# Performance work log

Measured on AMD Instinct MI355X. Metric: run time of the kernel, lower is better.

Reference implementation:

```python
import jax, jax.numpy as jnp
import numpy as np

V, E, H, N, B, T_CAP = 10000, 2048, 512, 98, 32, 61


def setup_inputs() -> dict:
    key = jax.random.key(0)
    ks = jax.random.split(key, 24)
    p = lambda k, shape: jax.random.normal(k, shape, dtype=jnp.float32) * 0.02
    inp = {
        "img_features": jax.random.normal(ks[0], (B, N, E), dtype=jnp.float32),
        "captions": jax.random.randint(ks[1], (B, T_CAP), 0, V),
        "emb": p(ks[2], (V, H)),
        "W_init_h": p(ks[3], (H, E)), "b_init_h": jnp.zeros((H,), jnp.float32),
        "W_init_c": p(ks[4], (H, E)), "b_init_c": jnp.zeros((H,), jnp.float32),
        "W_U": p(ks[5], (H, H)), "b_U": jnp.zeros((H,), jnp.float32),
        "W_att": p(ks[6], (H, E)), "b_att": jnp.zeros((H,), jnp.float32),
        "W_v": p(ks[7], (1, H)), "b_v": jnp.zeros((1,), jnp.float32),
        "W_fb": p(ks[8], (E, H)), "b_fb": jnp.zeros((E,), jnp.float32),
        "W_ih": p(ks[9], (4 * H, H + E)), "b_ih": jnp.zeros((4 * H,), jnp.float32),
        "W_hh": p(ks[10], (4 * H, H)), "b_hh": jnp.zeros((4 * H,), jnp.float32),
        "W_out": p(ks[11], (V, H)), "b_out": jnp.zeros((V,), jnp.float32),
    }
    return inp


def reference(img_features, captions, emb, W_init_h, b_init_h, W_init_c, b_init_c,
              W_U, b_U, W_att, b_att, W_v, b_v, W_fb, b_fb,
              W_ih, b_ih, W_hh, b_hh, W_out, b_out):
    # training-mode forward: max_timespan = caption_len - 1; dropout as identity (eval-style determinism)
    T = captions.shape[1] - 1
    avg = img_features.mean(axis=1)  # [B, E]
    h = jnp.tanh(avg @ W_init_h.T + b_init_h)  # [B, H]
    c = jnp.tanh(avg @ W_init_c.T + b_init_c)
    # Embeddings with sqrt(d_model) scaling
    emb_seq = emb[captions] * jnp.sqrt(jnp.float32(emb.shape[1]))  # [B, T_cap, H]
    # W_s is timestep-invariant: hoist out of loop (same math)
    Ws = jnp.einsum('bne,he->bnh', img_features, W_att) + b_att  # [B, N, H]

    def step(carry, emb_t):
        h, c = carry
        att = jnp.tanh(Ws + (h @ W_U.T + b_U)[:, None, :])       # [B, N, H]
        e = jnp.einsum('bnh,h->bn', att, W_v[0]) + b_v[0]        # [B, N]
        alpha = jax.nn.softmax(e, axis=1)
        context = jnp.einsum('bne,bn->be', img_features, alpha)  # [B, E]
        gate = jax.nn.sigmoid(h @ W_fb.T + b_fb)                 # [B, E]
        x = jnp.concatenate([emb_t, gate * context], axis=1)     # [B, H+E]
        gates = x @ W_ih.T + b_ih + h @ W_hh.T + b_hh            # [B, 4H]
        i_, f_, g_, o_ = jnp.split(gates, 4, axis=1)             # torch LSTMCell gate order
        c2 = jax.nn.sigmoid(f_) * c + jax.nn.sigmoid(i_) * jnp.tanh(g_)
        h2 = jax.nn.sigmoid(o_) * jnp.tanh(c2)
        pred = h2 @ W_out.T + b_out                              # [B, V]
        return (h2, c2), pred

    emb_steps = jnp.swapaxes(emb_seq[:, :T], 0, 1)  # [T, B, H]
    (_, _), preds = jax.lax.scan(step, (h, c), emb_steps)
    return jnp.swapaxes(preds, 0, 1)  # [B, T, V]
```

## Files before the change

### kernel.cpp

```cpp
#include <hip/hip_runtime.h>
#include <hip/hip_bf16.h>

#define BB   32
#define NN   98
#define EE   2048
#define HH   512
#define VV   10000
#define TT   60
#define TCAP 61

typedef unsigned short u16;
typedef __attribute__((ext_vector_type(8))) short bh8;
typedef __attribute__((ext_vector_type(4))) float f32x4;

__device__ __forceinline__ float bsf(unsigned s) {
    union { unsigned u; float f; } w; w.u = s << 16; return w.f;
}
__device__ __forceinline__ u16 f2bu(float f) {
    union { float f; unsigned u; } v; v.f = f;
    unsigned u = v.u;
    u = u + 0x7fffu + ((u >> 16) & 1u);
    return (u16)(u >> 16);
}
__device__ __forceinline__ bh8 ld8(const u16* p) {
    return *reinterpret_cast<const bh8*>(p);
}
__device__ __forceinline__ float sigm(float x) {
    return __builtin_amdgcn_rcpf(1.0f + exp2f(-1.4426950408889634f * x));
}
__device__ __forceinline__ float tanh_(float x) {
    return 1.0f - 2.0f * __builtin_amdgcn_rcpf(1.0f + exp2f(2.885390081777927f * x));
}

__global__ __launch_bounds__(256) void k_conv(
    const float* __restrict__ src, u16* __restrict__ dst)
{
    int i = blockIdx.x * 256 + threadIdx.x;
    float4 v = reinterpret_cast<const float4*>(src)[i];
    ushort4 o;
    o.x = f2bu(v.x); o.y = f2bu(v.y); o.z = f2bu(v.z); o.w = f2bu(v.w);
    reinterpret_cast<ushort4*>(dst)[i] = o;
}

__global__ __launch_bounds__(256) void k_init1(
    const float* __restrict__ img, const int* __restrict__ caps,
    const float* __restrict__ emb, u16* __restrict__ avg_bf, u16* __restrict__ emb_all)
{
    int bid = blockIdx.x, tid = threadIdx.x;
    if (bid < 256) {
        int b = bid >> 3, et = bid & 7;
        int ec = et * 256 + tid;
        const float* p = img + (size_t)(b * NN) * EE + ec;
        float s = 0.f;
        for (int n = 0; n < NN; ++n) s += p[(size_t)n * EE];
        avg_bf[b * EE + ec] = f2bu(s * (1.0f / 98.0f));
    } else {
        int eb = bid - 256;
        for (int r8 = 0; r8 < 8; ++r8) {
            int row = eb * 8 + r8;
            int t = row >> 5, b = row & 31;
            int cap = caps[b * TCAP + t];
            const float* src = emb + (size_t)cap * HH;
            u16* dst = emb_all + (size_t)row * HH;
            for (int c = tid; c < HH; c += 256)
                dst[c] = f2bu(src[c] * 22.627416997969522f);
        }
    }
}

__global__ __launch_bounds__(256) void k_init2(
    const u16* __restrict__ avg_bf,
    const u16* __restrict__ Wh_bf, const float* __restrict__ b_h,
    const u16* __restrict__ Wc_bf, const float* __restrict__ b_c,
    u16* __restrict__ h_all, float* __restrict__ c_ws)
{
    __shared__ float red[4][2][64][4];
    int ot = blockIdx.x, tid = threadIdx.x;
    int w = tid >> 6, lane = tid & 63, quad = lane >> 4, l16 = lane & 15;
    int o = ot * 16 + l16;
    const u16* wrow = (o < HH) ? (Wh_bf + (size_t)o * EE) : (Wc_bf + (size_t)(o - HH) * EE);
    f32x4 acc[2]; acc[0] = {0,0,0,0}; acc[1] = {0,0,0,0};
    for (int c = w * 16; c < w * 16 + 16; ++c) {
        int k = c * 32 + quad * 8;
        bh8 b8 = ld8(wrow + k);
        for (int mt = 0; mt < 2; ++mt) {
            bh8 a8 = ld8(avg_bf + (size_t)(mt * 16 + l16) * EE + k);
            acc[mt] = __builtin_amdgcn_mfma_f32_16x16x32_bf16(a8, b8, acc[mt], 0, 0, 0);
        }
    }
    for (int mt = 0; mt < 2; ++mt)
        for (int r = 0; r < 4; ++r) red[w][mt][lane][r] = acc[mt][r];
    __syncthreads();
    for (int idx = tid; idx < 512; idx += 256) {
        int mg = idx >> 4, nn2 = idx & 15;
        int mt = mg >> 4, m = mg & 15;
        int sl = nn2 + 16 * (m >> 2), rg = m & 3;
        float v = red[0][mt][sl][rg] + red[1][mt][sl][rg] + red[2][mt][sl][rg] + red[3][mt][sl][rg];
        int oo = ot * 16 + nn2, b = mg;
        if (oo < HH)
            h_all[(size_t)b * HH + oo] = f2bu(tanh_(v + b_h[oo]));
        else
            c_ws[b * HH + (oo - HH)] = tanh_(v + b_c[oo - HH]);
    }
}

__global__ __launch_bounds__(256) void k_ws(
    const u16* __restrict__ img_bf, const u16* __restrict__ Watt_bf,
    const float* __restrict__ b_att, u16* __restrict__ Ws_bf)
{
    int bid = blockIdx.x, tid = threadIdx.x;
    int mt = bid >> 4, nt = bid & 15;
    int w = tid >> 6, lane = tid & 63, quad = lane >> 4, l16 = lane & 15;
    int rowA = mt * 64 + w * 16 + l16;
    f32x4 acc[2]; acc[0] = {0,0,0,0}; acc[1] = {0,0,0,0};
    const u16* arow = img_bf + (size_t)rowA * EE;
    for (int c = 0; c < 64; ++c) {
        int k = c * 32 + quad * 8;
        bh8 a8 = ld8(arow + k);
        for (int s = 0; s < 2; ++s) {
            bh8 b8 = ld8(Watt_bf + (size_t)(nt * 32 + s * 16 + l16) * EE + k);
            acc[s] = __builtin_amdgcn_mfma_f32_16x16x32_bf16(a8, b8, acc[s], 0, 0, 0);
        }
    }
    for (int s = 0; s < 2; ++s)
        for (int r = 0; r < 4; ++r) {
            int m = quad * 4 + r;
            int row = mt * 64 + w * 16 + m;
            int col = nt * 32 + s * 16 + l16;
            Ws_bf[(size_t)row * HH + col] = f2bu(acc[s][r] + b_att[col]);
        }
}

__global__ __launch_bounds__(256) void k_c(
    const u16* __restrict__ h_all, int tIn,
    const u16* __restrict__ WU_bf, const float* __restrict__ b_U,
    const u16* __restrict__ Wfb_bf, const float* __restrict__ b_fb,
    float* __restrict__ Wu_ws, float* __restrict__ gate_ws)
{
    __shared__ float red[4][2][64][4];
    int ot = blockIdx.x, tid = threadIdx.x;
    int w = tid >> 6, lane = tid & 63, quad = lane >> 4, l16 = lane & 15;
    int o = ot * 16 + l16;
    const u16* wrow = (o < HH) ? (WU_bf + (size_t)o * HH) : (Wfb_bf + (size_t)(o - HH) * HH);
    const u16* hbase = h_all + (size_t)tIn * BB * HH;
    f32x4 acc[2]; acc[0] = {0,0,0,0}; acc[1] = {0,0,0,0};
    for (int c = w * 4; c < w * 4 + 4; ++c) {
        int k = c * 32 + quad * 8;
        bh8 b8 = ld8(wrow + k);
        for (int mt = 0; mt < 2; ++mt) {
            bh8 a8 = ld8(hbase + (size_t)(mt * 16 + l16) * HH + k);
            acc[mt] = __builtin_amdgcn_mfma_f32_16x16x32_bf16(a8, b8, acc[mt], 0, 0, 0);
        }
    }
    for (int mt = 0; mt < 2; ++mt)
        for (int r = 0; r < 4; ++r) red[w][mt][lane][r] = acc[mt][r];
    __syncthreads();
    for (int idx = tid; idx < 512; idx += 256) {
        int mg = idx >> 4, nn2 = idx & 15;
        int mt = mg >> 4, m = mg & 15;
        int sl = nn2 + 16 * (m >> 2), rg = m & 3;
        float v = red[0][mt][sl][rg] + red[1][mt][sl][rg] + red[2][mt][sl][rg] + red[3][mt][sl][rg];
        int oo = ot * 16 + nn2, b = mg;
        if (oo < HH)
            Wu_ws[b * HH + oo] = v + b_U[oo];
        else
            gate_ws[b * EE + (oo - HH)] = sigm(v + b_fb[oo - HH]);
    }
}

__global__ __launch_bounds__(256) void k_a(
    const float* __restrict__ img, const u16* __restrict__ Ws_bf,
    const float* __restrict__ Wu_ws, const float* __restrict__ gate_ws,
    const float* __restrict__ W_v, const float* __restrict__ b_v,
    u16* __restrict__ xctx)
{
    __shared__ float e_sh[NN];
    __shared__ float a_sh[NN];
    int bid = blockIdx.x, tid = threadIdx.x;
    int b = bid >> 2, et = bid & 3;
    int w = tid >> 6, lane = tid & 63;
    float wu[8], wv[8];
    {
        const float* wup = Wu_ws + b * HH + lane * 8;
        const float* wvp = W_v + lane * 8;
        #pragma unroll
        for (int j = 0; j < 8; ++j) { wu[j] = wup[j]; wv[j] = wvp[j]; }
    }
    for (int n = w; n < NN; n += 4) {
        bh8 ws8 = ld8(Ws_bf + (size_t)(b * NN + n) * HH + lane * 8);
        float acc = 0.f;
        #pragma unroll
        for (int j = 0; j < 8; ++j) acc += wv[j] * tanh_(bsf((u16)ws8[j]) + wu[j]);
        #pragma unroll
        for (int off = 32; off > 0; off >>= 1) acc += __shfl_down(acc, off, 64);
        if (lane == 0) e_sh[n] = acc + b_v[0];
    }
    __syncthreads();
    if (tid < 64) {
        float e0 = e_sh[tid];
        float e1 = (tid + 64 < NN) ? e_sh[tid + 64] : -1e30f;
        float m = fmaxf(e0, e1);
        #pragma unroll
        for (int off = 32; off > 0; off >>= 1) m = fmaxf(m, __shfl_xor(m, off, 64));
        const float L2E = 1.4426950408889634f;
        float x0 = exp2f((e0 - m) * L2E);
        float x1 = (tid + 64 < NN) ? exp2f((e1 - m) * L2E) : 0.f;
        float s = x0 + x1;
        #pragma unroll
        for (int off = 32; off > 0; off >>= 1) s += __shfl_xor(s, off, 64);
        float inv = __builtin_amdgcn_rcpf(s);
        a_sh[tid] = x0 * inv;
        if (tid + 64 < NN) a_sh[tid + 64] = x1 * inv;
    }
    __syncthreads();
    int ec = et * 512 + tid * 2;
    const float* ip = img + (size_t)b * NN * EE + ec;
    float c0 = 0.f, c1 = 0.f;
    for (int n = 0; n < NN; ++n) {
        float2 u = *reinterpret_cast<const float2*>(ip + (size_t)n * EE);
        float a = a_sh[n];
        c0 = fmaf(a, u.x, c0); c1 = fmaf(a, u.y, c1);
    }
    float g0 = gate_ws[b * EE + ec], g1 = gate_ws[b * EE + ec + 1];
    unsigned outw = ((unsigned)f2bu(g1 * c1) << 16) | (unsigned)f2bu(g0 * c0);
    *reinterpret_cast<unsigned*>(xctx + (size_t)b * EE + ec) = outw;
}

__global__ __launch_bounds__(256) void k_b(
    int t,
    const u16* __restrict__ emb_all, const u16* __restrict__ xctx,
    u16* h_all,
    const u16* __restrict__ Wih_bf, const float* __restrict__ b_ih,
    const u16* __restrict__ Whh_bf, const float* __restrict__ b_hh,
    float* __restrict__ c_ws)
{
    __shared__ float red[4][64][4];
    __shared__ float gsh[16][16];
    int bid = blockIdx.x, tid = threadIdx.x;
    int kt = bid & 127, mt = bid >> 7;
    int w = tid >> 6, lane = tid & 63, quad = lane >> 4, l16 = lane & 15;
    int brow = mt * 16 + l16;
    int j = kt * 4 + (l16 & 3) + HH * (l16 >> 2);
    const u16* embrow = emb_all + (size_t)(t * BB + brow) * HH;
    const u16* xrow   = xctx + (size_t)brow * EE;
    const u16* hrow   = h_all + (size_t)(t * BB + brow) * HH;
    const u16* wih    = Wih_bf + (size_t)j * (HH + EE);
    const u16* whh    = Whh_bf + (size_t)j * HH;
    f32x4 acc = {0,0,0,0};
    for (int c = w * 24; c < w * 24 + 24; ++c) {
        int k = c * 32 + quad * 8;
        bh8 a8, b8;
        if (c < 16)      a8 = ld8(embrow + k);
        else if (c < 80) a8 = ld8(xrow + (k - HH));
        else             a8 = ld8(hrow + (k - HH - EE));
        if (c < 80)      b8 = ld8(wih + k);
        else             b8 = ld8(whh + (k - HH - EE));
        acc = __builtin_amdgcn_mfma_f32_16x16x32_bf16(a8, b8, acc, 0, 0, 0);
    }
    for (int r = 0; r < 4; ++r) red[w][lane][r] = acc[r];
    __syncthreads();
    {
        int m = tid >> 4, nn2 = tid & 15;
        int sl = nn2 + 16 * (m >> 2), rg = m & 3;
        int jj = kt * 4 + (nn2 & 3) + HH * (nn2 >> 2);
        float v = red[0][sl][rg] + red[1][sl][rg] + red[2][sl][rg] + red[3][sl][rg]
                + b_ih[jj] + b_hh[jj];
        gsh[m][nn2] = v;
    }
    __syncthreads();
    if (tid < 64) {
        int m = tid >> 2, i = tid & 3;
        int b = mt * 16 + m, k = kt * 4 + i;
        float gi = gsh[m][i], gf = gsh[m][i + 4], gg = gsh[m][i + 8], go = gsh[m][i + 12];
        float cold = c_ws[b * HH + k];
        float c2 = sigm(gf) * cold + sigm(gi) * tanh_(gg);
        float h2 = sigm(go) * tanh_(c2);
        c_ws[b * HH + k] = c2;
        h_all[(size_t)((t + 1) * BB + b) * HH + k] = f2bu(h2);
    }
}

__global__ __launch_bounds__(256) void k_pred(
    const u16* __restrict__ h_all, const u16* __restrict__ Wout_bf,
    const float* __restrict__ b_out, float* __restrict__ out)
{
    int bid = blockIdx.x, tid = threadIdx.x;
    int mt = bid / 79, vt = bid % 79;
    int w = tid >> 6, lane = tid & 63, quad = lane >> 4, l16 = lane & 15;
    f32x4 acc[8][2];
    for (int mi = 0; mi < 8; ++mi) for (int s = 0; s < 2; ++s) acc[mi][s] = {0,0,0,0};
    int nact[2]; int vbase[2];
    for (int s = 0; s < 2; ++s) {
        int ntg = vt * 8 + 2 * w + s;
        nact[s] = (ntg < 625);
        vbase[s] = ntg * 16;
    }
    for (int c = 0; c < 16; ++c) {
        int k = c * 32 + quad * 8;
        bh8 b8[2];
        for (int s = 0; s < 2; ++s) if (nact[s])
            b8[s] = ld8(Wout_bf + (size_t)(vbase[s] + l16) * HH + k);
        for (int mi = 0; mi < 8; ++mi) {
            int row = 32 + mt * 128 + mi * 16 + l16;
            bh8 a8 = ld8(h_all + (size_t)row * HH + k);
            for (int s = 0; s < 2; ++s) if (nact[s])
                acc[mi][s] = __builtin_amdgcn_mfma_f32_16x16x32_bf16(a8, b8[s], acc[mi][s], 0, 0, 0);
        }
    }
    for (int s = 0; s < 2; ++s) if (nact[s]) {
        int v = vbase[s] + l16;
        float bo = b_out[v];
        for (int mi = 0; mi < 8; ++mi)
            for (int r = 0; r < 4; ++r) {
                int row = 32 + mt * 128 + mi * 16 + quad * 4 + r;
                int tt = (row >> 5) - 1, b = row & 31;
                out[(size_t)(b * TT + tt) * VV + v] = acc[mi][s][r] + bo;
            }
    }
}

extern "C" void kernel_launch(void* const* d_in, const int* in_sizes, int n_in,
                              void* d_out, int out_size, void* d_ws, size_t ws_size,
                              hipStream_t stream)
{
    const float* img      = (const float*)d_in[0];
    const int*   caps     = (const int*)d_in[1];
    const float* emb      = (const float*)d_in[2];
    const float* W_init_h = (const float*)d_in[3];
    const float* b_init_h = (const float*)d_in[4];
    const float* W_init_c = (const float*)d_in[5];
    const float* b_init_c = (const float*)d_in[6];
    const float* W_U      = (const float*)d_in[7];
    const float* b_U      = (const float*)d_in[8];
    const float* W_att    = (const float*)d_in[9];
    const float* b_att    = (const float*)d_in[10];
    const float* W_v      = (const float*)d_in[11];
    const float* b_v      = (const float*)d_in[12];
    const float* W_fb     = (const float*)d_in[13];
    const float* b_fb     = (const float*)d_in[14];
    const float* W_ih     = (const float*)d_in[15];
    const float* b_ih     = (const float*)d_in[16];
    const float* W_hh     = (const float*)d_in[17];
    const float* b_hh     = (const float*)d_in[18];
    const float* W_out    = (const float*)d_in[19];
    const float* b_out    = (const float*)d_in[20];
    float* out = (float*)d_out;

    char* ws = (char*)d_ws;
    u16*   img_bf  = (u16*)(ws);
    u16*   Watt_bf = (u16*)(ws + 12845056);
    u16*   Winh_bf = (u16*)(ws + 14942208);
    u16*   Winc_bf = (u16*)(ws + 17039360);
    u16*   WU_bf   = (u16*)(ws + 19136512);
    u16*   Wfb_bf  = (u16*)(ws + 19660800);
    u16*   Wih_bf  = (u16*)(ws + 21757952);
    u16*   Whh_bf  = (u16*)(ws + 32243712);
    u16*   Wout_bf = (u16*)(ws + 34340864);
    u16*   Ws_bf   = (u16*)(ws + 44580864);
    u16*   emb_all = (u16*)(ws + 47792128);
    u16*   h_all   = (u16*)(ws + 49758208);
    u16*   xctx    = (u16*)(ws + 51757056);
    u16*   avg_bf  = (u16*)(ws + 51888128);
    float* c_ws    = (float*)(ws + 52019200);
    float* Wu_ws   = (float*)(ws + 52084736);
    float* gate_ws = (float*)(ws + 52150272);

    k_conv<<<6272, 256, 0, stream>>>(img,      img_bf);
    k_conv<<<1024, 256, 0, stream>>>(W_att,    Watt_bf);
    k_conv<<<1024, 256, 0, stream>>>(W_init_h, Winh_bf);
    k_conv<<<1024, 256, 0, stream>>>(W_init_c, Winc_bf);
    k_conv<<< 256, 256, 0, stream>>>(W_U,      WU_bf);
    k_conv<<<1024, 256, 0, stream>>>(W_fb,     Wfb_bf);
    k_conv<<<5120, 256, 0, stream>>>(W_ih,     Wih_bf);
    k_conv<<<1024, 256, 0, stream>>>(W_hh,     Whh_bf);
    k_conv<<<5000, 256, 0, stream>>>(W_out,    Wout_bf);

    k_init1<<<496, 256, 0, stream>>>(img, caps, emb, avg_bf, emb_all);
    k_init2<<<64, 256, 0, stream>>>(avg_bf, Winh_bf, b_init_h, Winc_bf, b_init_c, h_all, c_ws);
    k_ws<<<784, 256, 0, stream>>>(img_bf, Watt_bf, b_att, Ws_bf);
    k_c<<<160, 256, 0, stream>>>(h_all, 0, WU_bf, b_U, Wfb_bf, b_fb, Wu_ws, gate_ws);
    for (int t = 0; t < TT; ++t) {
        k_a<<<128, 256, 0, stream>>>(img, Ws_bf, Wu_ws, gate_ws, W_v, b_v, xctx);
        k_b<<<256, 256, 0, stream>>>(t, emb_all, xctx, h_all, Wih_bf, b_ih, Whh_bf, b_hh, c_ws);
        if (t < TT - 1)
            k_c<<<160, 256, 0, stream>>>(h_all, t + 1, WU_bf, b_U, Wfb_bf, b_fb, Wu_ws, gate_ws);
    }
    k_pred<<<1185, 256, 0, stream>>>(h_all, Wout_bf, b_out, out);
}
```

Before: 2.669 ms.

## Fuse recurrent timestep kernels into one persistent kernel with grid barriers

Replaces the 179 per-timestep launches of k_a, k_b and k_c with a single persistent kernel of 256 blocks. The phases are separated by a software grid barrier built on an atomic counter and spin-waiting. The aim is to remove per-launch overhead and the gaps between launches on the sequential recurrence. In exchange it relies on all 256 blocks being co-resident, which needs 256 blocks on the GPU, and on correct memory fences; any block that is not resident would deadlock.

```diff
diff --git a/kernel.cpp b/kernel.cpp
--- a/kernel.cpp
+++ b/kernel.cpp
@@ -8,6 +8,7 @@
 #define VV   10000
 #define TT   60
 #define TCAP 61
+#define NBLK 256
 
 typedef unsigned short u16;
 typedef __attribute__((ext_vector_type(8))) short bh8;
@@ -131,152 +132,186 @@
         }
 }
 
-__global__ __launch_bounds__(256) void k_c(
-    const u16* __restrict__ h_all, int tIn,
+__global__ void k_zero(unsigned* cnt) { if (threadIdx.x == 0) *cnt = 0u; }
+
+__device__ __forceinline__ void gsync(unsigned* cnt, unsigned target) {
+    __syncthreads();
+    if (threadIdx.x == 0) {
+        __threadfence();
+        __hip_atomic_fetch_add(cnt, 1u, __ATOMIC_RELAXED, __HIP_MEMORY_SCOPE_AGENT);
+        unsigned v;
+        do {
+            __builtin_amdgcn_s_sleep(1);
+            v = __hip_atomic_load(cnt, __ATOMIC_RELAXED, __HIP_MEMORY_SCOPE_AGENT);
+        } while (v < target);
+        __threadfence();
+    }
+    __syncthreads();
+}
+
+__global__ __launch_bounds__(256, 2) void k_loop(
+    const float* __restrict__ img,
+    const u16* __restrict__ Ws_bf,
+    float* __restrict__ Wu_ws, float* __restrict__ gate_ws,
+    const float* __restrict__ W_v, const float* __restrict__ b_v,
+    u16* __restrict__ xctx,
+    const u16* __restrict__ emb_all,
+    u16* __restrict__ h_all,
+    const u16* __restrict__ Wih_bf, const float* __restrict__ b_ih,
+    const u16* __restrict__ Whh_bf, const float* __restrict__ b_hh,
+    float* __restrict__ c_ws,
     const u16* __restrict__ WU_bf, const float* __restrict__ b_U,
     const u16* __restrict__ Wfb_bf, const float* __restrict__ b_fb,
-    float* __restrict__ Wu_ws, float* __restrict__ gate_ws)
-{
-    __shared__ float red[4][2][64][4];
-    int ot = blockIdx.x, tid = threadIdx.x;
-    int w = tid >> 6, lane = tid & 63, quad = lane >> 4, l16 = lane & 15;
-    int o = ot * 16 + l16;
-    const u16* wrow = (o < HH) ? (WU_bf + (size_t)o * HH) : (Wfb_bf + (size_t)(o - HH) * HH);
-    const u16* hbase = h_all + (size_t)tIn * BB * HH;
-    f32x4 acc[2]; acc[0] = {0,0,0,0}; acc[1] = {0,0,0,0};
-    for (int c = w * 4; c < w * 4 + 4; ++c) {
-        int k = c * 32 + quad * 8;
-        bh8 b8 = ld8(wrow + k);
-        for (int mt = 0; mt < 2; ++mt) {
-            bh8 a8 = ld8(hbase + (size_t)(mt * 16 + l16) * HH + k);
-            acc[mt] = __builtin_amdgcn_mfma_f32_16x16x32_bf16(a8, b8, acc[mt], 0, 0, 0);
-        }
-    }
-    for (int mt = 0; mt < 2; ++mt)
-        for (int r = 0; r < 4; ++r) red[w][mt][lane][r] = acc[mt][r];
-    __syncthreads();
-    for (int idx = tid; idx < 512; idx += 256) {
-        int mg = idx >> 4, nn2 = idx & 15;
-        int mt = mg >> 4, m = mg & 15;
-        int sl = nn2 + 16 * (m >> 2), rg = m & 3;
-        float v = red[0][mt][sl][rg] + red[1][mt][sl][rg] + red[2][mt][sl][rg] + red[3][mt][sl][rg];
-        int oo = ot * 16 + nn2, b = mg;
-        if (oo < HH)
-            Wu_ws[b * HH + oo] = v + b_U[oo];
-        else
-            gate_ws[b * EE + (oo - HH)] = sigm(v + b_fb[oo - HH]);
-    }
-}
-
-__global__ __launch_bounds__(256) void k_a(
-    const float* __restrict__ img, const u16* __restrict__ Ws_bf,
-    const float* __restrict__ Wu_ws, const float* __restrict__ gate_ws,
-    const float* __restrict__ W_v, const float* __restrict__ b_v,
-    u16* __restrict__ xctx)
-{
+    unsigned* cnt)
+{
+    __shared__ float redC[4][2][64][4];
+    __shared__ float redB[4][64][4];
+    __shared__ float gsh[16][16];
     __shared__ float e_sh[NN];
     __shared__ float a_sh[NN];
-    int bid = blockIdx.x, tid = threadIdx.x;
-    int b = bid >> 2, et = bid & 3;
-    int w = tid >> 6, lane = tid & 63;
-    float wu[8], wv[8];
-    {
-        const float* wup = Wu_ws + b * HH + lane * 8;
-        const float* wvp = W_v + lane * 8;
-        #pragma unroll
-        for (int j = 0; j < 8; ++j) { wu[j] = wup[j]; wv[j] = wvp[j]; }
-    }
-    for (int n = w; n < NN; n += 4) {
-        bh8 ws8 = ld8(Ws_bf + (size_t)(b * NN + n) * HH + lane * 8);
-        float acc = 0.f;
-        #pragma unroll
-        for (int j = 0; j < 8; ++j) acc += wv[j] * tanh_(bsf((u16)ws8[j]) + wu[j]);
-        #pragma unroll
-        for (int off = 32; off > 0; off >>= 1) acc += __shfl_down(acc, off, 64);
-        if (lane == 0) e_sh[n] = acc + b_v[0];
-    }
-    __syncthreads();
-    if (tid < 64) {
-        float e0 = e_sh[tid];
-        float e1 = (tid + 64 < NN) ? e_sh[tid + 64] : -1e30f;
-        float m = fmaxf(e0, e1);
-        #pragma unroll
-        for (int off = 32; off > 0; off >>= 1) m = fmaxf(m, __shfl_xor(m, off, 64));
-        const float L2E = 1.4426950408889634f;
-        float x0 = exp2f((e0 - m) * L2E);
-        float x1 = (tid + 64 < NN) ? exp2f((e1 - m) * L2E) : 0.f;
-        float s = x0 + x1;
-        #pragma unroll
-        for (int off = 32; off > 0; off >>= 1) s += __shfl_xor(s, off, 64);
-        float inv = __builtin_amdgcn_rcpf(s);
-        a_sh[tid] = x0 * inv;
-        if (tid + 64 < NN) a_sh[tid + 64] = x1 * inv;
-    }
-    __syncthreads();
-    int ec = et * 512 + tid * 2;
-    const float* ip = img + (size_t)b * NN * EE + ec;
-    float c0 = 0.f, c1 = 0.f;
-    for (int n = 0; n < NN; ++n) {
-        float2 u = *reinterpret_cast<const float2*>(ip + (size_t)n * EE);
-        float a = a_sh[n];
-        c0 = fmaf(a, u.x, c0); c1 = fmaf(a, u.y, c1);
-    }
-    float g0 = gate_ws[b * EE + ec], g1 = gate_ws[b * EE + ec + 1];
-    unsigned outw = ((unsigned)f2bu(g1 * c1) << 16) | (unsigned)f2bu(g0 * c0);
-    *reinterpret_cast<unsigned*>(xctx + (size_t)b * EE + ec) = outw;
-}
-
-__global__ __launch_bounds__(256) void k_b(
-    int t,
-    const u16* __restrict__ emb_all, const u16* __restrict__ xctx,
-    u16* h_all,
-    const u16* __restrict__ Wih_bf, const float* __restrict__ b_ih,
-    const u16* __restrict__ Whh_bf, const float* __restrict__ b_hh,
-    float* __restrict__ c_ws)
-{
-    __shared__ float red[4][64][4];
-    __shared__ float gsh[16][16];
-    int bid = blockIdx.x, tid = threadIdx.x;
-    int kt = bid & 127, mt = bid >> 7;
-    int w = tid >> 6, lane = tid & 63, quad = lane >> 4, l16 = lane & 15;
-    int brow = mt * 16 + l16;
-    int j = kt * 4 + (l16 & 3) + HH * (l16 >> 2);
-    const u16* embrow = emb_all + (size_t)(t * BB + brow) * HH;
-    const u16* xrow   = xctx + (size_t)brow * EE;
-    const u16* hrow   = h_all + (size_t)(t * BB + brow) * HH;
-    const u16* wih    = Wih_bf + (size_t)j * (HH + EE);
-    const u16* whh    = Whh_bf + (size_t)j * HH;
-    f32x4 acc = {0,0,0,0};
-    for (int c = w * 24; c < w * 24 + 24; ++c) {
-        int k = c * 32 + quad * 8;
-        bh8 a8, b8;
-        if (c < 16)      a8 = ld8(embrow + k);
-        else if (c < 80) a8 = ld8(xrow + (k - HH));
-        else             a8 = ld8(hrow + (k - HH - EE));
-        if (c < 80)      b8 = ld8(wih + k);
-        else             b8 = ld8(whh + (k - HH - EE));
-        acc = __builtin_amdgcn_mfma_f32_16x16x32_bf16(a8, b8, acc, 0, 0, 0);
-    }
-    for (int r = 0; r < 4; ++r) red[w][lane][r] = acc[r];
-    __syncthreads();
-    {
-        int m = tid >> 4, nn2 = tid & 15;
-        int sl = nn2 + 16 * (m >> 2), rg = m & 3;
-        int jj = kt * 4 + (nn2 & 3) + HH * (nn2 >> 2);
-        float v = red[0][sl][rg] + red[1][sl][rg] + red[2][sl][rg] + red[3][sl][rg]
-                + b_ih[jj] + b_hh[jj];
-        gsh[m][nn2] = v;
-    }
-    __syncthreads();
-    if (tid < 64) {
-        int m = tid >> 2, i = tid & 3;
-        int b = mt * 16 + m, k = kt * 4 + i;
-        float gi = gsh[m][i], gf = gsh[m][i + 4], gg = gsh[m][i + 8], go = gsh[m][i + 12];
-        float cold = c_ws[b * HH + k];
-        float c2 = sigm(gf) * cold + sigm(gi) * tanh_(gg);
-        float h2 = sigm(go) * tanh_(c2);
-        c_ws[b * HH + k] = c2;
-        h_all[(size_t)((t + 1) * BB + b) * HH + k] = f2bu(h2);
+
+    const int bid = blockIdx.x, tid = threadIdx.x;
+    const int w = tid >> 6, lane = tid & 63, quad = lane >> 4, l16 = lane & 15;
+    unsigned snc = 0;
+
+    auto phaseC = [&](int tIn) {
+        if (bid < 160) {
+            int ot = bid;
+            int o = ot * 16 + l16;
+            const u16* wrow = (o < HH) ? (WU_bf + (size_t)o * HH) : (Wfb_bf + (size_t)(o - HH) * HH);
+            const u16* hbase = h_all + (size_t)tIn * BB * HH;
+            f32x4 acc[2]; acc[0] = {0,0,0,0}; acc[1] = {0,0,0,0};
+            for (int c = w * 4; c < w * 4 + 4; ++c) {
+                int k = c * 32 + quad * 8;
+                bh8 b8 = ld8(wrow + k);
+                for (int mt = 0; mt < 2; ++mt) {
+                    bh8 a8 = ld8(hbase + (size_t)(mt * 16 + l16) * HH + k);
+                    acc[mt] = __builtin_amdgcn_mfma_f32_16x16x32_bf16(a8, b8, acc[mt], 0, 0, 0);
+                }
+            }
+            for (int mt = 0; mt < 2; ++mt)
+                for (int r = 0; r < 4; ++r) redC[w][mt][lane][r] = acc[mt][r];
+            __syncthreads();
+            for (int idx = tid; idx < 512; idx += 256) {
+                int mg = idx >> 4, nn2 = idx & 15;
+                int mt = mg >> 4, m = mg & 15;
+                int sl = nn2 + 16 * (m >> 2), rg = m & 3;
+                float v = redC[0][mt][sl][rg] + redC[1][mt][sl][rg]
+                        + redC[2][mt][sl][rg] + redC[3][mt][sl][rg];
+                int oo = ot * 16 + nn2, b = mg;
+                if (oo < HH)
+                    Wu_ws[b * HH + oo] = v + b_U[oo];
+                else
+                    gate_ws[b * EE + (oo - HH)] = sigm(v + b_fb[oo - HH]);
+            }
+        }
+    };
+
+    auto phaseA = [&]() {
+        if (bid < 128) {
+            int b = bid >> 2, et = bid & 3;
+            float wu[8], wv[8];
+            {
+                const float* wup = Wu_ws + b * HH + lane * 8;
+                const float* wvp = W_v + lane * 8;
+                #pragma unroll
+                for (int j = 0; j < 8; ++j) { wu[j] = wup[j]; wv[j] = wvp[j]; }
+            }
+            for (int n = w; n < NN; n += 4) {
+                bh8 ws8 = ld8(Ws_bf + (size_t)(b * NN + n) * HH + lane * 8);
+                float acc = 0.f;
+                #pragma unroll
+                for (int j = 0; j < 8; ++j) acc += wv[j] * tanh_(bsf((u16)ws8[j]) + wu[j]);
+                #pragma unroll
+                for (int off = 32; off > 0; off >>= 1) acc += __shfl_down(acc, off, 64);
+                if (lane == 0) e_sh[n] = acc + b_v[0];
+            }
+            __syncthreads();
+            if (tid < 64) {
+                float e0 = e_sh[tid];
+                float e1 = (tid + 64 < NN) ? e_sh[tid + 64] : -1e30f;
+                float m = fmaxf(e0, e1);
+                #pragma unroll
+                for (int off = 32; off > 0; off >>= 1) m = fmaxf(m, __shfl_xor(m, off, 64));
+                const float L2E = 1.4426950408889634f;
+                float x0 = exp2f((e0 - m) * L2E);
+                float x1 = (tid + 64 < NN) ? exp2f((e1 - m) * L2E) : 0.f;
+                float s = x0 + x1;
+                #pragma unroll
+                for (int off = 32; off > 0; off >>= 1) s += __shfl_xor(s, off, 64);
+                float inv = __builtin_amdgcn_rcpf(s);
+                a_sh[tid] = x0 * inv;
+                if (tid + 64 < NN) a_sh[tid + 64] = x1 * inv;
+            }
+            __syncthreads();
+            int ec = et * 512 + tid * 2;
+            const float* ip = img + (size_t)b * NN * EE + ec;
+            float c0 = 0.f, c1 = 0.f;
+            for (int n = 0; n < NN; ++n) {
+                float2 u = *reinterpret_cast<const float2*>(ip + (size_t)n * EE);
+                float a = a_sh[n];
+                c0 = fmaf(a, u.x, c0); c1 = fmaf(a, u.y, c1);
+            }
+            float g0 = gate_ws[b * EE + ec], g1 = gate_ws[b * EE + ec + 1];
+            unsigned outw = ((unsigned)f2bu(g1 * c1) << 16) | (unsigned)f2bu(g0 * c0);
+            *reinterpret_cast<unsigned*>(xctx + (size_t)b * EE + ec) = outw;
+        }
+    };
+
+    auto phaseB = [&](int t) {
+        int kt = bid & 127, mt = bid >> 7;
+        int brow = mt * 16 + l16;
+        int j = kt * 4 + (l16 & 3) + HH * (l16 >> 2);
+        const u16* embrow = emb_all + (size_t)(t * BB + brow) * HH;
+        const u16* xrow   = xctx + (size_t)brow * EE;
+        const u16* hrow   = h_all + (size_t)(t * BB + brow) * HH;
+        const u16* wih    = Wih_bf + (size_t)j * (HH + EE);
+        const u16* whh    = Whh_bf + (size_t)j * HH;
+        f32x4 acc = {0,0,0,0};
+        for (int c = w * 24; c < w * 24 + 24; ++c) {
+            int k = c * 32 + quad * 8;
+            bh8 a8, b8;
+            if (c < 16)      a8 = ld8(embrow + k);
+            else if (c < 80) a8 = ld8(xrow + (k - HH));
+            else             a8 = ld8(hrow + (k - HH - EE));
+            if (c < 80)      b8 = ld8(wih + k);
+            else             b8 = ld8(whh + (k - HH - EE));
+            acc = __builtin_amdgcn_mfma_f32_16x16x32_bf16(a8, b8, acc, 0, 0, 0);
+        }
+        for (int r = 0; r < 4; ++r) redB[w][lane][r] = acc[r];
+        __syncthreads();
+        {
+            int m = tid >> 4, nn2 = tid & 15;
+            int sl = nn2 + 16 * (m >> 2), rg = m & 3;
+            int jj = kt * 4 + (nn2 & 3) + HH * (nn2 >> 2);
+            float v = redB[0][sl][rg] + redB[1][sl][rg] + redB[2][sl][rg] + redB[3][sl][rg]
+                    + b_ih[jj] + b_hh[jj];
+            gsh[m][nn2] = v;
+        }
+        __syncthreads();
+        if (tid < 64) {
+            int m = tid >> 2, i = tid & 3;
+            int b = mt * 16 + m, k = kt * 4 + i;
+            float gi = gsh[m][i], gf = gsh[m][i + 4], gg = gsh[m][i + 8], go = gsh[m][i + 12];
+            float cold = c_ws[b * HH + k];
+            float c2 = sigm(gf) * cold + sigm(gi) * tanh_(gg);
+            float h2 = sigm(go) * tanh_(c2);
+            c_ws[b * HH + k] = c2;
+            h_all[(size_t)((t + 1) * BB + b) * HH + k] = f2bu(h2);
+        }
+    };
+
+    phaseC(0);
+    gsync(cnt, ++snc * NBLK);
+    for (int t = 0; t < TT; ++t) {
+        phaseA();
+        gsync(cnt, ++snc * NBLK);
+        phaseB(t);
+        gsync(cnt, ++snc * NBLK);
+        if (t < TT - 1) {
+            phaseC(t + 1);
+            gsync(cnt, ++snc * NBLK);
+        }
     }
 }
 
@@ -364,6 +399,7 @@
     float* c_ws    = (float*)(ws + 52019200);
     float* Wu_ws   = (float*)(ws + 52084736);
     float* gate_ws = (float*)(ws + 52150272);
+    unsigned* sync_cnt = (unsigned*)(ws + 52412416);
 
     k_conv<<<6272, 256, 0, stream>>>(img,      img_bf);
     k_conv<<<1024, 256, 0, stream>>>(W_att,    Watt_bf);
@@ -378,12 +414,11 @@
     k_init1<<<496, 256, 0, stream>>>(img, caps, emb, avg_bf, emb_all);
     k_init2<<<64, 256, 0, stream>>>(avg_bf, Winh_bf, b_init_h, Winc_bf, b_init_c, h_all, c_ws);
     k_ws<<<784, 256, 0, stream>>>(img_bf, Watt_bf, b_att, Ws_bf);
-    k_c<<<160, 256, 0, stream>>>(h_all, 0, WU_bf, b_U, Wfb_bf, b_fb, Wu_ws, gate_ws);
-    for (int t = 0; t < TT; ++t) {
-        k_a<<<128, 256, 0, stream>>>(img, Ws_bf, Wu_ws, gate_ws, W_v, b_v, xctx);
-        k_b<<<256, 256, 0, stream>>>(t, emb_all, xctx, h_all, Wih_bf, b_ih, Whh_bf, b_hh, c_ws);
-        if (t < TT - 1)
-            k_c<<<160, 256, 0, stream>>>(h_all, t + 1, WU_bf, b_U, Wfb_bf, b_fb, Wu_ws, gate_ws);
-    }
+
+    k_zero<<<1, 64, 0, stream>>>(sync_cnt);
+    k_loop<<<NBLK, 256, 0, stream>>>(img, Ws_bf, Wu_ws, gate_ws, W_v, b_v, xctx,
+                                     emb_all, h_all, Wih_bf, b_ih, Whh_bf, b_hh, c_ws,
+                                     WU_bf, b_U, Wfb_bf, b_fb, sync_cnt);
+
     k_pred<<<1185, 256, 0, stream>>>(h_all, Wout_bf, b_out, out);
 }
```

After: 8.070 ms. 3.02x slower.
